# Optimization experiments

Hardware: AMD Instinct MI355X
Metric: run time of the kernel (lower is better)

## Reference

```python
import jax, jax.numpy as jnp
import numpy as np


def setup_inputs() -> dict:
    key = jax.random.key(0)
    B, S, N, D = 4, 512, 8, 256
    ks = jax.random.split(key, 5)
    s = 0.02
    inp = {"x": jax.random.normal(ks[0], (B, S, N, D), jnp.float32)}
    for k, name in zip(ks[1:], ["Wq", "Wk", "Wv", "Wo"]):
        inp[name] = jax.random.normal(k, (D, D), jnp.float32) * s
    for name in ["bq", "bk", "bv", "bo"]:
        inp[name] = jnp.zeros((D,), jnp.float32)
    inp["gamma"] = jnp.ones((D,), jnp.float32)
    inp["beta"] = jnp.zeros((D,), jnp.float32)
    inp["num_heads"] = 8
    return inp


def reference(x, Wq, bq, Wk, bk, Wv, bv, Wo, bo, gamma, beta, num_heads):
    B, S, N, D = x.shape
    H = num_heads
    hd = D // H
    # sinusoidal positional encoding: even dims sin, odd dims cos
    pos = jnp.arange(S, dtype=jnp.float32)[:, None]                      # (S,1)
    div = jnp.exp(jnp.arange(0, D, 2, dtype=jnp.float32) * (-np.log(10000.0) / D))
    ang = pos * div                                                       # (S, D/2)
    pe = jnp.stack([jnp.sin(ang), jnp.cos(ang)], axis=-1).reshape(S, D)   # (S, D)
    x_pos = x + pe[None, :, None, :]                                      # (B,S,N,D)
    # fold sensors into batch: (B*N, S, D)
    xr = x_pos.transpose(0, 2, 1, 3).reshape(B * N, S, D)

    def proj(W, b):
        y = xr @ W.T + b                                                  # torch Linear
        return y.reshape(B * N, S, H, hd).transpose(0, 2, 1, 3)          # (BN,H,S,hd)

    Q, K, V = proj(Wq, bq), proj(Wk, bk), proj(Wv, bv)
    scores = jnp.einsum('bhqd,bhkd->bhqk', Q, K) / np.sqrt(hd)            # (BN,H,S,S)
    causal = jnp.tril(jnp.ones((S, S), dtype=bool))
    scores = jnp.where(causal[None, None], scores, jnp.float32(-1e9))
    attn = jax.nn.softmax(scores, axis=-1)                                # dropout = eval mode
    out = jnp.einsum('bhqk,bhkd->bhqd', attn, V)                          # (BN,H,S,hd)
    out = out.transpose(0, 2, 1, 3).reshape(B * N, S, D)
    out = out @ Wo.T + bo
    out = out.reshape(B, N, S, D).transpose(0, 2, 1, 3)                   # (B,S,N,D)
    y = out + x
    mu = jnp.mean(y, axis=-1, keepdims=True)
    var = jnp.var(y, axis=-1, keepdims=True)
    return (y - mu) / jnp.sqrt(var + 1e-5) * gamma + beta
```

## Files before the change

### kernel.cpp

```cpp
#include <hip/hip_runtime.h>
#include <hip/hip_bf16.h>
#include <math.h>

#define B_   4
#define S_   512
#define N_   8
#define D_   256
#define H_   8
#define HD_  32
#define BN_  32
#define MTOT (BN_ * S_)

typedef __attribute__((ext_vector_type(8))) short short8;
typedef __attribute__((ext_vector_type(4))) short short4v;
typedef __attribute__((ext_vector_type(4))) float floatx4;

#define QSCALE 0.25503468f

__device__ __forceinline__ float bf2f(short u) {
    union { unsigned u; float f; } c;
    c.u = ((unsigned)(unsigned short)u) << 16;
    return c.f;
}
__device__ __forceinline__ unsigned short f2bf(float f) {
    union { float f; unsigned u; } c; c.f = f;
    unsigned lsb = (c.u >> 16) & 1u;
    c.u += 0x7fffu + lsb;
    return (unsigned short)(c.u >> 16);
}
__device__ __forceinline__ unsigned short f2bf_ru(float f) {
    union { float f; unsigned u; } c; c.f = f;
    return (unsigned short)((c.u + 0x8000u) >> 16);
}
__device__ __forceinline__ float fexp2(float x) {
    float r; asm("v_exp_f32 %0, %1" : "=v"(r) : "v"(x)); return r;
}

__global__ __launch_bounds__(256) void prep_kernel(const float* __restrict__ x,
                                                   const float* __restrict__ Wq,
                                                   const float* __restrict__ Wk,
                                                   const float* __restrict__ Wv,
                                                   const float* __restrict__ Wo,
                                                   unsigned short* __restrict__ xpos,
                                                   unsigned short* __restrict__ wdst) {
    int bid = blockIdx.x;
    if (bid < 4096) {
        int idx4 = bid * 256 + threadIdx.x;
        int d0 = (idx4 << 2) & (D_ - 1);
        int s  = (idx4 >> 6) & (S_ - 1);
        int bn = idx4 >> 15;
        int b = bn >> 3, n = bn & 7;
        floatx4 xv = *(const floatx4*)(x + ((((size_t)b * S_ + s) * N_ + n) << 8) + d0);
        const float cfreq = -9.210340371976184f / 256.0f;
        float f0 = __expf((float)d0 * cfreq);
        float f1 = __expf((float)(d0 + 2) * cfreq);
        float a0 = (float)s * f0, a1 = (float)s * f1;
        short4v o;
        o[0] = (short)f2bf(xv[0] + __sinf(a0));
        o[1] = (short)f2bf(xv[1] + __cosf(a0));
        o[2] = (short)f2bf(xv[2] + __sinf(a1));
        o[3] = (short)f2bf(xv[3] + __cosf(a1));
        *(short4v*)(xpos + ((size_t)idx4 << 2)) = o;
    } else {
        int idx = (bid - 4096) * 256 + threadIdx.x;
        int which = idx >> 16, off = idx & 65535;
        const float* W = (which == 0) ? Wq : (which == 1) ? Wk : (which == 2) ? Wv : Wo;
        wdst[idx] = f2bf(W[off]);
    }
}

__global__ __launch_bounds__(256) void gemm_qkv_kernel(const unsigned short* __restrict__ A,
                                                       const unsigned short* __restrict__ W,
                                                       const float* __restrict__ bq,
                                                       const float* __restrict__ bk,
                                                       const float* __restrict__ bv,
                                                       unsigned short* __restrict__ Qb,
                                                       unsigned short* __restrict__ Kb,
                                                       unsigned short* __restrict__ Vt) {
    int wv = threadIdx.x >> 6, lane = threadIdx.x & 63;
    int col = lane & 15, quad = lane >> 4;
    int m_w = blockIdx.x * 128 + (wv >> 1) * 64;
    int n_w = blockIdx.y * 128 + (wv & 1) * 64;

    const short8* Ap = (const short8*)(A + (size_t)(m_w + col) * 256 + quad * 8);
    const short8* Bp = (const short8*)(W + (size_t)(n_w + col) * 256 + quad * 8);

    floatx4 acc[4][4] = {};
#pragma unroll
    for (int kk = 0; kk < 8; ++kk) {
        short8 a[4], b[4];
#pragma unroll
        for (int t = 0; t < 4; ++t) {
            a[t] = Ap[t * 512 + kk * 4];
            b[t] = Bp[t * 512 + kk * 4];
        }
#pragma unroll
        for (int mt = 0; mt < 4; ++mt)
#pragma unroll
            for (int nt = 0; nt < 4; ++nt)
                acc[mt][nt] = __builtin_amdgcn_mfma_f32_16x16x32_bf16(a[mt], b[nt], acc[mt][nt], 0, 0, 0);
    }

    int sel = blockIdx.y >> 1;
    const float* bias = (sel == 0) ? bq : (sel == 1) ? bk : bv;
#pragma unroll
    for (int nt = 0; nt < 4; ++nt) {
        int c = n_w + nt * 16 + col - sel * 256;
        float bv_ = bias[c];
#pragma unroll
        for (int mt = 0; mt < 4; ++mt) {
            int m0 = m_w + mt * 16 + quad * 4;
            if (sel == 2) {
                int bn = m0 >> 9, s0 = m0 & (S_ - 1);
                short4v pack;
#pragma unroll
                for (int r = 0; r < 4; ++r) pack[r] = (short)f2bf(acc[mt][nt][r] + bv_);
                *(short4v*)(Vt + (((size_t)((bn << 8) + c)) << 9) + s0) = pack;
            } else if (sel == 0) {
#pragma unroll
                for (int r = 0; r < 4; ++r)
                    Qb[((size_t)(m0 + r) << 8) | c] = f2bf((acc[mt][nt][r] + bv_) * QSCALE);
            } else {
#pragma unroll
                for (int r = 0; r < 4; ++r)
                    Kb[((size_t)(m0 + r) << 8) | c] = f2bf(acc[mt][nt][r] + bv_);
            }
        }
    }
}

#define PSTR 40
__global__ __launch_bounds__(256) void fattn_kernel(const unsigned short* __restrict__ Q,
                                                    const unsigned short* __restrict__ K,
                                                    const unsigned short* __restrict__ Vt,
                                                    unsigned short* __restrict__ O) {
    __shared__ unsigned short Plds[4][16 * PSTR];
    int wv = threadIdx.x >> 6, lane = threadIdx.x & 63;
    int col = lane & 15, quad = lane >> 4;
    int bnh  = blockIdx.x & 255;
    int qblk = blockIdx.x >> 8;
    int bn = bnh >> 3, h = bnh & 7;
    int q0 = qblk * 64 + wv * 16;

    unsigned short* P = &Plds[wv][0];

    short8 qfrag = *(const short8*)(Q + (((size_t)(bn * S_ + q0 + col)) << 8) + h * HD_ + quad * 8);
    const unsigned short* Kbase = K + (((size_t)(bn * S_)) << 8) + h * HD_ + quad * 8;
    const unsigned short* Vbase = Vt + (((size_t)(bnh * HD_)) << 9) + quad * 8;

    float l = 0.f;
    floatx4 o0 = {0.f, 0.f, 0.f, 0.f};
    floatx4 o1 = {0.f, 0.f, 0.f, 0.f};
    int lastk = q0 >> 5;

    for (int kt = 0; kt <= lastk; ++kt) {
        int k0 = kt * 32;
        short8 kf0 = *(const short8*)(Kbase + ((size_t)(k0 + col) << 8));
        short8 kf1 = *(const short8*)(Kbase + ((size_t)(k0 + 16 + col) << 8));
        floatx4 z = {0.f, 0.f, 0.f, 0.f};
        floatx4 st0 = __builtin_amdgcn_mfma_f32_16x16x32_bf16(kf0, qfrag, z, 0, 0, 0);
        floatx4 st1 = __builtin_amdgcn_mfma_f32_16x16x32_bf16(kf1, qfrag, z, 0, 0, 0);

        if (kt == lastk) {
            int qg = q0 + col;
#pragma unroll
            for (int r = 0; r < 4; ++r) {
                if (k0 + quad * 4 + r > qg)      st0[r] = -1e30f;
                if (k0 + 16 + quad * 4 + r > qg) st1[r] = -1e30f;
            }
        }

        float p[8]; float ts = 0.f;
#pragma unroll
        for (int r = 0; r < 4; ++r) {
            p[r]     = fexp2(st0[r]);
            p[4 + r] = fexp2(st1[r]);
            ts += p[r] + p[4 + r];
        }
        ts += __shfl_xor(ts, 16);
        ts += __shfl_xor(ts, 32);
        l += ts;

        short4v pk0, pk1;
#pragma unroll
        for (int r = 0; r < 4; ++r) {
            pk0[r] = (short)f2bf_ru(p[r]);
            pk1[r] = (short)f2bf_ru(p[4 + r]);
        }
        *(short4v*)&P[col * PSTR + quad * 4]      = pk0;
        *(short4v*)&P[col * PSTR + 16 + quad * 4] = pk1;
        asm volatile("s_waitcnt lgkmcnt(0)" ::: "memory");
        short8 pfrag = *(const short8*)&P[col * PSTR + quad * 8];

        short8 vf0 = *(const short8*)(Vbase + ((size_t)col << 9) + k0);
        short8 vf1 = *(const short8*)(Vbase + ((size_t)(16 + col) << 9) + k0);
        o0 = __builtin_amdgcn_mfma_f32_16x16x32_bf16(vf0, pfrag, o0, 0, 0, 0);
        o1 = __builtin_amdgcn_mfma_f32_16x16x32_bf16(vf1, pfrag, o1, 0, 0, 0);
    }

    float inv = 1.0f / l;
    unsigned short* Op = O + (((size_t)(bn * S_ + q0 + col)) << 8) + h * HD_;
    short4v s0v, s1v;
#pragma unroll
    for (int r = 0; r < 4; ++r) {
        s0v[r] = (short)f2bf(o0[r] * inv);
        s1v[r] = (short)f2bf(o1[r] * inv);
    }
    *(short4v*)(Op + quad * 4)      = s0v;
    *(short4v*)(Op + 16 + quad * 4) = s1v;
}

__global__ __launch_bounds__(256) void gemm_o_ln_kernel(const unsigned short* __restrict__ A,
                                                        const unsigned short* __restrict__ W,
                                                        const float* __restrict__ bo,
                                                        const float* __restrict__ x,
                                                        const float* __restrict__ gamma,
                                                        const float* __restrict__ beta,
                                                        float* __restrict__ out) {
    __shared__ float lsum[4][64];
    __shared__ float lss[4][64];
    __shared__ float lmu[64];
    __shared__ float lrs[64];

    int wv = threadIdx.x >> 6, lane = threadIdx.x & 63;
    int col = lane & 15, quad = lane >> 4;
    int m_b = blockIdx.x * 64;
    int n_w = wv * 64;

    const short8* Ap = (const short8*)(A + (size_t)(m_b + col) * 256 + quad * 8);
    const short8* Bp = (const short8*)(W + (size_t)(n_w + col) * 256 + quad * 8);

    floatx4 acc[4][4] = {};
#pragma unroll
    for (int kk = 0; kk < 8; ++kk) {
        short8 a[4], b[4];
#pragma unroll
        for (int t = 0; t < 4; ++t) {
            a[t] = Ap[t * 512 + kk * 4];
            b[t] = Bp[t * 512 + kk * 4];
        }
#pragma unroll
        for (int mt = 0; mt < 4; ++mt)
#pragma unroll
            for (int nt = 0; nt < 4; ++nt)
                acc[mt][nt] = __builtin_amdgcn_mfma_f32_16x16x32_bf16(a[mt], b[nt], acc[mt][nt], 0, 0, 0);
    }

    int bn = m_b >> 9, s0 = m_b & (S_ - 1);
    int b_ = bn >> 3, n_ = bn & 7;
    const float* xrow = x + ((((size_t)b_ * S_ + s0) * N_ + n_) << 8);
    float* orow = out + ((((size_t)b_ * S_ + s0) * N_ + n_) << 8);

    float psum[4][4] = {};
    float pss[4][4]  = {};
#pragma unroll
    for (int nt = 0; nt < 4; ++nt) {
        int c = n_w + nt * 16 + col;
        float bv_ = bo[c];
#pragma unroll
        for (int mt = 0; mt < 4; ++mt) {
            int sl = mt * 16 + quad * 4;
#pragma unroll
            for (int r = 0; r < 4; ++r) {
                float y = acc[mt][nt][r] + bv_ + xrow[(size_t)(sl + r) * 2048 + c];
                acc[mt][nt][r] = y;
                psum[mt][r] += y;
                pss[mt][r]  += y * y;
            }
        }
    }
#pragma unroll
    for (int off = 8; off >= 1; off >>= 1) {
#pragma unroll
        for (int mt = 0; mt < 4; ++mt)
#pragma unroll
            for (int r = 0; r < 4; ++r) {
                psum[mt][r] += __shfl_xor(psum[mt][r], off);
                pss[mt][r]  += __shfl_xor(pss[mt][r], off);
            }
    }
    if (col == 0) {
#pragma unroll
        for (int mt = 0; mt < 4; ++mt)
#pragma unroll
            for (int r = 0; r < 4; ++r) {
                lsum[wv][mt * 16 + quad * 4 + r] = psum[mt][r];
                lss[wv][mt * 16 + quad * 4 + r]  = pss[mt][r];
            }
    }
    __syncthreads();
    if (threadIdx.x < 64) {
        int row = threadIdx.x;
        float s  = lsum[0][row] + lsum[1][row] + lsum[2][row] + lsum[3][row];
        float ss = lss[0][row] + lss[1][row] + lss[2][row] + lss[3][row];
        float mu = s * (1.0f / 256.0f);
        float var = ss * (1.0f / 256.0f) - mu * mu;
        lmu[row] = mu;
        lrs[row] = rsqrtf(var + 1e-5f);
    }
    __syncthreads();

#pragma unroll
    for (int nt = 0; nt < 4; ++nt) {
        int c = n_w + nt * 16 + col;
        float g  = gamma[c];
        float be = beta[c];
#pragma unroll
        for (int mt = 0; mt < 4; ++mt) {
            int sl = mt * 16 + quad * 4;
#pragma unroll
            for (int r = 0; r < 4; ++r)
                orow[(size_t)(sl + r) * 2048 + c] =
                    (acc[mt][nt][r] - lmu[sl + r]) * lrs[sl + r] * g + be;
        }
    }
}

extern "C" void kernel_launch(void* const* d_in, const int* in_sizes, int n_in,
                              void* d_out, int out_size, void* d_ws, size_t ws_size,
                              hipStream_t stream) {
    const float* x     = (const float*)d_in[0];
    const float* Wq    = (const float*)d_in[1];
    const float* Wk    = (const float*)d_in[2];
    const float* Wv    = (const float*)d_in[3];
    const float* Wo    = (const float*)d_in[4];
    const float* bq    = (const float*)d_in[5];
    const float* bk    = (const float*)d_in[6];
    const float* bv    = (const float*)d_in[7];
    const float* bo    = (const float*)d_in[8];
    const float* gamma = (const float*)d_in[9];
    const float* beta  = (const float*)d_in[10];

    char* w = (char*)d_ws;
    const size_t SZ = (size_t)MTOT * D_ * 2;
    unsigned short* xpos = (unsigned short*)(w);
    unsigned short* Qb   = (unsigned short*)(w + SZ);
    unsigned short* Kb   = (unsigned short*)(w + 2 * SZ);
    unsigned short* Vt   = (unsigned short*)(w + 3 * SZ);
    unsigned short* Ab   = (unsigned short*)(w + 4 * SZ);
    unsigned short* Wbf  = (unsigned short*)(w + 5 * SZ);

    prep_kernel<<<5120, 256, 0, stream>>>(x, Wq, Wk, Wv, Wo, xpos, Wbf);
    gemm_qkv_kernel<<<dim3(128, 6), 256, 0, stream>>>(xpos, Wbf, bq, bk, bv, Qb, Kb, Vt);
    fattn_kernel<<<2048, 256, 0, stream>>>(Qb, Kb, Vt, Ab);
    gemm_o_ln_kernel<<<256, 256, 0, stream>>>(Ab, Wbf + 3 * 65536, bo, x, gamma, beta, (float*)d_out);
}
```

Baseline: 167.7 us.

## Fuse all stages into one cooperative persistent kernel with grid syncs

Replaces the four separate launches (prep, QKV GEMM, flash attention, O-proj+LayerNorm) with a single cooperative kernel of 256 blocks of 1024 threads, separated by grid-wide syncs. Work is remapped per wave: the QKV GEMM uses 64x48 wave tiles, and attention pairs query tile i with tile 31-i so causal work is balanced across waves. The aim is to remove launch gaps and tail effects between stages. In exchange it adds grid-sync cost, and 1024-thread blocks limit occupancy and register budget.

New measurement: 280.0 us. 1.67x slower.

```diff
diff --git a/kernel.cpp b/kernel.cpp
--- a/kernel.cpp
+++ b/kernel.cpp
@@ -1,6 +1,9 @@
 #include <hip/hip_runtime.h>
 #include <hip/hip_bf16.h>
+#include <hip/hip_cooperative_groups.h>
 #include <math.h>
+
+namespace cg = cooperative_groups;
 
 #define B_   4
 #define S_   512
@@ -17,11 +20,6 @@
 
 #define QSCALE 0.25503468f
 
-__device__ __forceinline__ float bf2f(short u) {
-    union { unsigned u; float f; } c;
-    c.u = ((unsigned)(unsigned short)u) << 16;
-    return c.f;
-}
 __device__ __forceinline__ unsigned short f2bf(float f) {
     union { float f; unsigned u; } c; c.f = f;
     unsigned lsb = (c.u >> 16) & 1u;
@@ -36,282 +34,263 @@
     float r; asm("v_exp_f32 %0, %1" : "=v"(r) : "v"(x)); return r;
 }
 
-__global__ __launch_bounds__(256) void prep_kernel(const float* __restrict__ x,
-                                                   const float* __restrict__ Wq,
-                                                   const float* __restrict__ Wk,
-                                                   const float* __restrict__ Wv,
-                                                   const float* __restrict__ Wo,
-                                                   unsigned short* __restrict__ xpos,
-                                                   unsigned short* __restrict__ wdst) {
-    int bid = blockIdx.x;
-    if (bid < 4096) {
-        int idx4 = bid * 256 + threadIdx.x;
-        int d0 = (idx4 << 2) & (D_ - 1);
-        int s  = (idx4 >> 6) & (S_ - 1);
-        int bn = idx4 >> 15;
-        int b = bn >> 3, n = bn & 7;
-        floatx4 xv = *(const floatx4*)(x + ((((size_t)b * S_ + s) * N_ + n) << 8) + d0);
+#define PSTR 40
+
+__global__ __launch_bounds__(1024) void mega_kernel(
+        const float* __restrict__ x,
+        const float* __restrict__ Wq, const float* __restrict__ Wk,
+        const float* __restrict__ Wv, const float* __restrict__ Wo,
+        const float* __restrict__ bq, const float* __restrict__ bk,
+        const float* __restrict__ bv, const float* __restrict__ bo,
+        const float* __restrict__ gamma, const float* __restrict__ beta,
+        unsigned short* __restrict__ xpos, unsigned short* __restrict__ Wbf,
+        unsigned short* __restrict__ Qb, unsigned short* __restrict__ Kb,
+        unsigned short* __restrict__ Vt, unsigned short* __restrict__ Ab,
+        float* __restrict__ out) {
+    cg::grid_group grid = cg::this_grid();
+    __shared__ __align__(16) char smem[16 * 16 * PSTR * 2];
+
+    const int wid  = threadIdx.x >> 6;
+    const int lane = threadIdx.x & 63;
+    const int col  = lane & 15, quad = lane >> 4;
+    const int gw   = blockIdx.x * 16 + wid;
+    const int tid  = blockIdx.x * 1024 + threadIdx.x;
+
+    {
         const float cfreq = -9.210340371976184f / 256.0f;
-        float f0 = __expf((float)d0 * cfreq);
-        float f1 = __expf((float)(d0 + 2) * cfreq);
-        float a0 = (float)s * f0, a1 = (float)s * f1;
-        short4v o;
-        o[0] = (short)f2bf(xv[0] + __sinf(a0));
-        o[1] = (short)f2bf(xv[1] + __cosf(a0));
-        o[2] = (short)f2bf(xv[2] + __sinf(a1));
-        o[3] = (short)f2bf(xv[3] + __cosf(a1));
-        *(short4v*)(xpos + ((size_t)idx4 << 2)) = o;
-    } else {
-        int idx = (bid - 4096) * 256 + threadIdx.x;
-        int which = idx >> 16, off = idx & 65535;
+        for (int idx4 = tid; idx4 < (MTOT * D_) / 4; idx4 += 262144) {
+            int d0 = (idx4 << 2) & (D_ - 1);
+            int s  = (idx4 >> 6) & (S_ - 1);
+            int bn = idx4 >> 15;
+            int b = bn >> 3, n = bn & 7;
+            floatx4 xv = *(const floatx4*)(x + ((((size_t)b * S_ + s) * N_ + n) << 8) + d0);
+            float f0 = __expf((float)d0 * cfreq);
+            float f1 = __expf((float)(d0 + 2) * cfreq);
+            float a0 = (float)s * f0, a1 = (float)s * f1;
+            short4v o;
+            o[0] = (short)f2bf(xv[0] + __sinf(a0));
+            o[1] = (short)f2bf(xv[1] + __cosf(a0));
+            o[2] = (short)f2bf(xv[2] + __sinf(a1));
+            o[3] = (short)f2bf(xv[3] + __cosf(a1));
+            *(short4v*)(xpos + ((size_t)idx4 << 2)) = o;
+        }
+        int which = tid >> 16, off = tid & 65535;
         const float* W = (which == 0) ? Wq : (which == 1) ? Wk : (which == 2) ? Wv : Wo;
-        wdst[idx] = f2bf(W[off]);
+        Wbf[tid] = f2bf(W[off]);
     }
-}
-
-__global__ __launch_bounds__(256) void gemm_qkv_kernel(const unsigned short* __restrict__ A,
-                                                       const unsigned short* __restrict__ W,
-                                                       const float* __restrict__ bq,
-                                                       const float* __restrict__ bk,
-                                                       const float* __restrict__ bv,
-                                                       unsigned short* __restrict__ Qb,
-                                                       unsigned short* __restrict__ Kb,
-                                                       unsigned short* __restrict__ Vt) {
-    int wv = threadIdx.x >> 6, lane = threadIdx.x & 63;
-    int col = lane & 15, quad = lane >> 4;
-    int m_w = blockIdx.x * 128 + (wv >> 1) * 64;
-    int n_w = blockIdx.y * 128 + (wv & 1) * 64;
-
-    const short8* Ap = (const short8*)(A + (size_t)(m_w + col) * 256 + quad * 8);
-    const short8* Bp = (const short8*)(W + (size_t)(n_w + col) * 256 + quad * 8);
-
-    floatx4 acc[4][4] = {};
-#pragma unroll
-    for (int kk = 0; kk < 8; ++kk) {
-        short8 a[4], b[4];
-#pragma unroll
-        for (int t = 0; t < 4; ++t) {
-            a[t] = Ap[t * 512 + kk * 4];
-            b[t] = Bp[t * 512 + kk * 4];
-        }
-#pragma unroll
-        for (int mt = 0; mt < 4; ++mt)
+    grid.sync();
+
+    {
+        int m_idx = gw >> 4, n_idx = gw & 15;
+        int m_w = m_idx * 64, n_w = n_idx * 48;
+
+        const short8* Ap = (const short8*)(xpos + (size_t)(m_w + col) * 256 + quad * 8);
+        const short8* Bp = (const short8*)(Wbf + (size_t)(n_w + col) * 256 + quad * 8);
+
+        floatx4 acc[4][3] = {};
+#pragma unroll
+        for (int kk = 0; kk < 8; ++kk) {
+            short8 a[4], b[3];
+#pragma unroll
+            for (int t = 0; t < 4; ++t) a[t] = Ap[t * 512 + kk * 4];
+#pragma unroll
+            for (int t = 0; t < 3; ++t) b[t] = Bp[t * 512 + kk * 4];
+#pragma unroll
+            for (int mt = 0; mt < 4; ++mt)
+#pragma unroll
+                for (int nt = 0; nt < 3; ++nt)
+                    acc[mt][nt] = __builtin_amdgcn_mfma_f32_16x16x32_bf16(a[mt], b[nt], acc[mt][nt], 0, 0, 0);
+        }
+#pragma unroll
+        for (int nt = 0; nt < 3; ++nt) {
+            int cgl = n_w + nt * 16 + col;
+            int sel = cgl >> 8;
+            int c   = cgl & 255;
+            float bv_ = ((sel == 0) ? bq : (sel == 1) ? bk : bv)[c];
+#pragma unroll
+            for (int mt = 0; mt < 4; ++mt) {
+                int m0 = m_w + mt * 16 + quad * 4;
+                if (sel == 2) {
+                    int bn = m0 >> 9, s0 = m0 & (S_ - 1);
+                    short4v pack;
+#pragma unroll
+                    for (int r = 0; r < 4; ++r) pack[r] = (short)f2bf(acc[mt][nt][r] + bv_);
+                    *(short4v*)(Vt + (((size_t)((bn << 8) + c)) << 9) + s0) = pack;
+                } else if (sel == 0) {
+#pragma unroll
+                    for (int r = 0; r < 4; ++r)
+                        Qb[((size_t)(m0 + r) << 8) | c] = f2bf((acc[mt][nt][r] + bv_) * QSCALE);
+                } else {
+#pragma unroll
+                    for (int r = 0; r < 4; ++r)
+                        Kb[((size_t)(m0 + r) << 8) | c] = f2bf(acc[mt][nt][r] + bv_);
+                }
+            }
+        }
+    }
+    grid.sync();
+
+    {
+        unsigned short* P = (unsigned short*)smem + wid * (16 * PSTR);
+        int bnh = gw & 255;
+        int bn = bnh >> 3, h = bnh & 7;
+        int qts[2] = { gw >> 8, 31 - (gw >> 8) };
+        const unsigned short* Kbase = Kb + (((size_t)(bn * S_)) << 8) + h * HD_ + quad * 8;
+        const unsigned short* Vbase = Vt + (((size_t)(bnh * HD_)) << 9) + quad * 8;
+
+#pragma unroll
+        for (int ui = 0; ui < 2; ++ui) {
+            int q0 = qts[ui] * 16;
+            short8 qfrag = *(const short8*)(Qb + (((size_t)(bn * S_ + q0 + col)) << 8) + h * HD_ + quad * 8);
+            float l = 0.f;
+            floatx4 o0 = {0.f, 0.f, 0.f, 0.f};
+            floatx4 o1 = {0.f, 0.f, 0.f, 0.f};
+            int lastk = q0 >> 5;
+
+            for (int kt = 0; kt <= lastk; ++kt) {
+                int k0 = kt * 32;
+                short8 kf0 = *(const short8*)(Kbase + ((size_t)(k0 + col) << 8));
+                short8 kf1 = *(const short8*)(Kbase + ((size_t)(k0 + 16 + col) << 8));
+                floatx4 z = {0.f, 0.f, 0.f, 0.f};
+                floatx4 st0 = __builtin_amdgcn_mfma_f32_16x16x32_bf16(kf0, qfrag, z, 0, 0, 0);
+                floatx4 st1 = __builtin_amdgcn_mfma_f32_16x16x32_bf16(kf1, qfrag, z, 0, 0, 0);
+
+                if (kt == lastk) {
+                    int qg = q0 + col;
+#pragma unroll
+                    for (int r = 0; r < 4; ++r) {
+                        if (k0 + quad * 4 + r > qg)      st0[r] = -1e30f;
+                        if (k0 + 16 + quad * 4 + r > qg) st1[r] = -1e30f;
+                    }
+                }
+                float p[8]; float ts = 0.f;
+#pragma unroll
+                for (int r = 0; r < 4; ++r) {
+                    p[r]     = fexp2(st0[r]);
+                    p[4 + r] = fexp2(st1[r]);
+                    ts += p[r] + p[4 + r];
+                }
+                ts += __shfl_xor(ts, 16);
+                ts += __shfl_xor(ts, 32);
+                l += ts;
+
+                short4v pk0, pk1;
+#pragma unroll
+                for (int r = 0; r < 4; ++r) {
+                    pk0[r] = (short)f2bf_ru(p[r]);
+                    pk1[r] = (short)f2bf_ru(p[4 + r]);
+                }
+                *(short4v*)&P[col * PSTR + quad * 4]      = pk0;
+                *(short4v*)&P[col * PSTR + 16 + quad * 4] = pk1;
+                asm volatile("s_waitcnt lgkmcnt(0)" ::: "memory");
+                short8 pfrag = *(const short8*)&P[col * PSTR + quad * 8];
+
+                short8 vf0 = *(const short8*)(Vbase + ((size_t)col << 9) + k0);
+                short8 vf1 = *(const short8*)(Vbase + ((size_t)(16 + col) << 9) + k0);
+                o0 = __builtin_amdgcn_mfma_f32_16x16x32_bf16(vf0, pfrag, o0, 0, 0, 0);
+                o1 = __builtin_amdgcn_mfma_f32_16x16x32_bf16(vf1, pfrag, o1, 0, 0, 0);
+            }
+
+            float inv = 1.0f / l;
+            unsigned short* Op = Ab + (((size_t)(bn * S_ + q0 + col)) << 8) + h * HD_;
+            short4v s0v, s1v;
+#pragma unroll
+            for (int r = 0; r < 4; ++r) {
+                s0v[r] = (short)f2bf(o0[r] * inv);
+                s1v[r] = (short)f2bf(o1[r] * inv);
+            }
+            *(short4v*)(Op + quad * 4)      = s0v;
+            *(short4v*)(Op + 16 + quad * 4) = s1v;
+        }
+    }
+    grid.sync();
+
+    {
+        float* lsum = (float*)smem;
+        float* lss  = (float*)smem + 256;
+        float* lmu  = (float*)smem + 512;
+        float* lrs  = (float*)smem + 576;
+
+        const unsigned short* Wo_bf = Wbf + 3 * 65536;
+        int g  = wid >> 2, cq = wid & 3;
+        int m_b = blockIdx.x * 64;
+        int m_w = m_b + g * 16;
+        int n_w = cq * 64;
+
+        const short8* Ap = (const short8*)(Ab + (size_t)(m_w + col) * 256 + quad * 8);
+        const short8* Bp = (const short8*)(Wo_bf + (size_t)(n_w + col) * 256 + quad * 8);
+
+        floatx4 acc[4] = {};
+#pragma unroll
+        for (int kk = 0; kk < 8; ++kk) {
+            short8 a = Ap[kk * 4];
+            short8 b[4];
+#pragma unroll
+            for (int t = 0; t < 4; ++t) b[t] = Bp[t * 512 + kk * 4];
 #pragma unroll
             for (int nt = 0; nt < 4; ++nt)
-                acc[mt][nt] = __builtin_amdgcn_mfma_f32_16x16x32_bf16(a[mt], b[nt], acc[mt][nt], 0, 0, 0);
-    }
-
-    int sel = blockIdx.y >> 1;
-    const float* bias = (sel == 0) ? bq : (sel == 1) ? bk : bv;
-#pragma unroll
-    for (int nt = 0; nt < 4; ++nt) {
-        int c = n_w + nt * 16 + col - sel * 256;
-        float bv_ = bias[c];
-#pragma unroll
-        for (int mt = 0; mt < 4; ++mt) {
-            int m0 = m_w + mt * 16 + quad * 4;
-            if (sel == 2) {
-                int bn = m0 >> 9, s0 = m0 & (S_ - 1);
-                short4v pack;
-#pragma unroll
-                for (int r = 0; r < 4; ++r) pack[r] = (short)f2bf(acc[mt][nt][r] + bv_);
-                *(short4v*)(Vt + (((size_t)((bn << 8) + c)) << 9) + s0) = pack;
-            } else if (sel == 0) {
-#pragma unroll
-                for (int r = 0; r < 4; ++r)
-                    Qb[((size_t)(m0 + r) << 8) | c] = f2bf((acc[mt][nt][r] + bv_) * QSCALE);
-            } else {
-#pragma unroll
-                for (int r = 0; r < 4; ++r)
-                    Kb[((size_t)(m0 + r) << 8) | c] = f2bf(acc[mt][nt][r] + bv_);
-            }
-        }
-    }
-}
-
-#define PSTR 40
-__global__ __launch_bounds__(256) void fattn_kernel(const unsigned short* __restrict__ Q,
-                                                    const unsigned short* __restrict__ K,
-                                                    const unsigned short* __restrict__ Vt,
-                                                    unsigned short* __restrict__ O) {
-    __shared__ unsigned short Plds[4][16 * PSTR];
-    int wv = threadIdx.x >> 6, lane = threadIdx.x & 63;
-    int col = lane & 15, quad = lane >> 4;
-    int bnh  = blockIdx.x & 255;
-    int qblk = blockIdx.x >> 8;
-    int bn = bnh >> 3, h = bnh & 7;
-    int q0 = qblk * 64 + wv * 16;
-
-    unsigned short* P = &Plds[wv][0];
-
-    short8 qfrag = *(const short8*)(Q + (((size_t)(bn * S_ + q0 + col)) << 8) + h * HD_ + quad * 8);
-    const unsigned short* Kbase = K + (((size_t)(bn * S_)) << 8) + h * HD_ + quad * 8;
-    const unsigned short* Vbase = Vt + (((size_t)(bnh * HD_)) << 9) + quad * 8;
-
-    float l = 0.f;
-    floatx4 o0 = {0.f, 0.f, 0.f, 0.f};
-    floatx4 o1 = {0.f, 0.f, 0.f, 0.f};
-    int lastk = q0 >> 5;
-
-    for (int kt = 0; kt <= lastk; ++kt) {
-        int k0 = kt * 32;
-        short8 kf0 = *(const short8*)(Kbase + ((size_t)(k0 + col) << 8));
-        short8 kf1 = *(const short8*)(Kbase + ((size_t)(k0 + 16 + col) << 8));
-        floatx4 z = {0.f, 0.f, 0.f, 0.f};
-        floatx4 st0 = __builtin_amdgcn_mfma_f32_16x16x32_bf16(kf0, qfrag, z, 0, 0, 0);
-        floatx4 st1 = __builtin_amdgcn_mfma_f32_16x16x32_bf16(kf1, qfrag, z, 0, 0, 0);
-
-        if (kt == lastk) {
-            int qg = q0 + col;
-#pragma unroll
-            for (int r = 0; r < 4; ++r) {
-                if (k0 + quad * 4 + r > qg)      st0[r] = -1e30f;
-                if (k0 + 16 + quad * 4 + r > qg) st1[r] = -1e30f;
-            }
-        }
-
-        float p[8]; float ts = 0.f;
-#pragma unroll
-        for (int r = 0; r < 4; ++r) {
-            p[r]     = fexp2(st0[r]);
-            p[4 + r] = fexp2(st1[r]);
-            ts += p[r] + p[4 + r];
-        }
-        ts += __shfl_xor(ts, 16);
-        ts += __shfl_xor(ts, 32);
-        l += ts;
-
-        short4v pk0, pk1;
-#pragma unroll
-        for (int r = 0; r < 4; ++r) {
-            pk0[r] = (short)f2bf_ru(p[r]);
-            pk1[r] = (short)f2bf_ru(p[4 + r]);
-        }
-        *(short4v*)&P[col * PSTR + quad * 4]      = pk0;
-        *(short4v*)&P[col * PSTR + 16 + quad * 4] = pk1;
-        asm volatile("s_waitcnt lgkmcnt(0)" ::: "memory");
-        short8 pfrag = *(const short8*)&P[col * PSTR + quad * 8];
-
-        short8 vf0 = *(const short8*)(Vbase + ((size_t)col << 9) + k0);
-        short8 vf1 = *(const short8*)(Vbase + ((size_t)(16 + col) << 9) + k0);
-        o0 = __builtin_amdgcn_mfma_f32_16x16x32_bf16(vf0, pfrag, o0, 0, 0, 0);
-        o1 = __builtin_amdgcn_mfma_f32_16x16x32_bf16(vf1, pfrag, o1, 0, 0, 0);
-    }
-
-    float inv = 1.0f / l;
-    unsigned short* Op = O + (((size_t)(bn * S_ + q0 + col)) << 8) + h * HD_;
-    short4v s0v, s1v;
-#pragma unroll
-    for (int r = 0; r < 4; ++r) {
-        s0v[r] = (short)f2bf(o0[r] * inv);
-        s1v[r] = (short)f2bf(o1[r] * inv);
-    }
-    *(short4v*)(Op + quad * 4)      = s0v;
-    *(short4v*)(Op + 16 + quad * 4) = s1v;
-}
-
-__global__ __launch_bounds__(256) void gemm_o_ln_kernel(const unsigned short* __restrict__ A,
-                                                        const unsigned short* __restrict__ W,
-                                                        const float* __restrict__ bo,
-                                                        const float* __restrict__ x,
-                                                        const float* __restrict__ gamma,
-                                                        const float* __restrict__ beta,
-                                                        float* __restrict__ out) {
-    __shared__ float lsum[4][64];
-    __shared__ float lss[4][64];
-    __shared__ float lmu[64];
-    __shared__ float lrs[64];
-
-    int wv = threadIdx.x >> 6, lane = threadIdx.x & 63;
-    int col = lane & 15, quad = lane >> 4;
-    int m_b = blockIdx.x * 64;
-    int n_w = wv * 64;
-
-    const short8* Ap = (const short8*)(A + (size_t)(m_b + col) * 256 + quad * 8);
-    const short8* Bp = (const short8*)(W + (size_t)(n_w + col) * 256 + quad * 8);
-
-    floatx4 acc[4][4] = {};
-#pragma unroll
-    for (int kk = 0; kk < 8; ++kk) {
-        short8 a[4], b[4];
-#pragma unroll
-        for (int t = 0; t < 4; ++t) {
-            a[t] = Ap[t * 512 + kk * 4];
-            b[t] = Bp[t * 512 + kk * 4];
-        }
-#pragma unroll
-        for (int mt = 0; mt < 4; ++mt)
-#pragma unroll
-            for (int nt = 0; nt < 4; ++nt)
-                acc[mt][nt] = __builtin_amdgcn_mfma_f32_16x16x32_bf16(a[mt], b[nt], acc[mt][nt], 0, 0, 0);
-    }
-
-    int bn = m_b >> 9, s0 = m_b & (S_ - 1);
-    int b_ = bn >> 3, n_ = bn & 7;
-    const float* xrow = x + ((((size_t)b_ * S_ + s0) * N_ + n_) << 8);
-    float* orow = out + ((((size_t)b_ * S_ + s0) * N_ + n_) << 8);
-
-    float psum[4][4] = {};
-    float pss[4][4]  = {};
-#pragma unroll
-    for (int nt = 0; nt < 4; ++nt) {
-        int c = n_w + nt * 16 + col;
-        float bv_ = bo[c];
-#pragma unroll
-        for (int mt = 0; mt < 4; ++mt) {
-            int sl = mt * 16 + quad * 4;
-#pragma unroll
-            for (int r = 0; r < 4; ++r) {
-                float y = acc[mt][nt][r] + bv_ + xrow[(size_t)(sl + r) * 2048 + c];
-                acc[mt][nt][r] = y;
-                psum[mt][r] += y;
-                pss[mt][r]  += y * y;
-            }
-        }
-    }
-#pragma unroll
-    for (int off = 8; off >= 1; off >>= 1) {
-#pragma unroll
-        for (int mt = 0; mt < 4; ++mt)
-#pragma unroll
-            for (int r = 0; r < 4; ++r) {
-                psum[mt][r] += __shfl_xor(psum[mt][r], off);
-                pss[mt][r]  += __shfl_xor(pss[mt][r], off);
-            }
-    }
-    if (col == 0) {
-#pragma unroll
-        for (int mt = 0; mt < 4; ++mt)
-#pragma unroll
-            for (int r = 0; r < 4; ++r) {
-                lsum[wv][mt * 16 + quad * 4 + r] = psum[mt][r];
-                lss[wv][mt * 16 + quad * 4 + r]  = pss[mt][r];
-            }
-    }
-    __syncthreads();
-    if (threadIdx.x < 64) {
-        int row = threadIdx.x;
-        float s  = lsum[0][row] + lsum[1][row] + lsum[2][row] + lsum[3][row];
-        float ss = lss[0][row] + lss[1][row] + lss[2][row] + lss[3][row];
-        float mu = s * (1.0f / 256.0f);
-        float var = ss * (1.0f / 256.0f) - mu * mu;
-        lmu[row] = mu;
-        lrs[row] = rsqrtf(var + 1e-5f);
-    }
-    __syncthreads();
-
-#pragma unroll
-    for (int nt = 0; nt < 4; ++nt) {
-        int c = n_w + nt * 16 + col;
-        float g  = gamma[c];
-        float be = beta[c];
-#pragma unroll
-        for (int mt = 0; mt < 4; ++mt) {
-            int sl = mt * 16 + quad * 4;
-#pragma unroll
-            for (int r = 0; r < 4; ++r)
-                orow[(size_t)(sl + r) * 2048 + c] =
-                    (acc[mt][nt][r] - lmu[sl + r]) * lrs[sl + r] * g + be;
+                acc[nt] = __builtin_amdgcn_mfma_f32_16x16x32_bf16(a, b[nt], acc[nt], 0, 0, 0);
+        }
+
+        int bn = m_b >> 9, s0 = m_b & (S_ - 1);
+        int b_ = bn >> 3, n_ = bn & 7;
+        const float* xrow = x + ((((size_t)b_ * S_ + s0) * N_ + n_) << 8);
+        float* orow = out + ((((size_t)b_ * S_ + s0) * N_ + n_) << 8);
+
+        float psum[4] = {}, pss[4] = {};
+#pragma unroll
+        for (int nt = 0; nt < 4; ++nt) {
+            int c = n_w + nt * 16 + col;
+            float bv_ = bo[c];
+#pragma unroll
+            for (int r = 0; r < 4; ++r) {
+                int sl = g * 16 + quad * 4 + r;
+                float y = acc[nt][r] + bv_ + xrow[(size_t)sl * 2048 + c];
+                acc[nt][r] = y;
+                psum[r] += y;
+                pss[r]  += y * y;
+            }
+        }
+#pragma unroll
+        for (int off = 8; off >= 1; off >>= 1) {
+#pragma unroll
+            for (int r = 0; r < 4; ++r) {
+                psum[r] += __shfl_xor(psum[r], off);
+                pss[r]  += __shfl_xor(pss[r], off);
+            }
+        }
+        if (col == 0) {
+#pragma unroll
+            for (int r = 0; r < 4; ++r) {
+                lsum[wid * 16 + quad * 4 + r] = psum[r];
+                lss[wid * 16 + quad * 4 + r]  = pss[r];
+            }
+        }
+        __syncthreads();
+        if (threadIdx.x < 64) {
+            int row = threadIdx.x;
+            int gg = row >> 4, rl = row & 15;
+            float s = 0.f, ss = 0.f;
+#pragma unroll
+            for (int q2 = 0; q2 < 4; ++q2) {
+                s  += lsum[(gg * 4 + q2) * 16 + rl];
+                ss += lss[(gg * 4 + q2) * 16 + rl];
+            }
+            float mu = s * (1.0f / 256.0f);
+            float var = ss * (1.0f / 256.0f) - mu * mu;
+            lmu[row] = mu;
+            lrs[row] = rsqrtf(var + 1e-5f);
+        }
+        __syncthreads();
+#pragma unroll
+        for (int nt = 0; nt < 4; ++nt) {
+            int c = n_w + nt * 16 + col;
+            float ga = gamma[c], be = beta[c];
+#pragma unroll
+            for (int r = 0; r < 4; ++r) {
+                int sl = g * 16 + quad * 4 + r;
+                orow[(size_t)sl * 2048 + c] = (acc[nt][r] - lmu[sl]) * lrs[sl] * ga + be;
+            }
         }
     }
 }
@@ -339,9 +318,10 @@
     unsigned short* Vt   = (unsigned short*)(w + 3 * SZ);
     unsigned short* Ab   = (unsigned short*)(w + 4 * SZ);
     unsigned short* Wbf  = (unsigned short*)(w + 5 * SZ);
-
-    prep_kernel<<<5120, 256, 0, stream>>>(x, Wq, Wk, Wv, Wo, xpos, Wbf);
-    gemm_qkv_kernel<<<dim3(128, 6), 256, 0, stream>>>(xpos, Wbf, bq, bk, bv, Qb, Kb, Vt);
-    fattn_kernel<<<2048, 256, 0, stream>>>(Qb, Kb, Vt, Ab);
-    gemm_o_ln_kernel<<<256, 256, 0, stream>>>(Ab, Wbf + 3 * 65536, bo, x, gamma, beta, (float*)d_out);
-}
+    float* outp = (float*)d_out;
+
+    void* args[] = { &x, &Wq, &Wk, &Wv, &Wo, &bq, &bk, &bv, &bo, &gamma, &beta,
+                     &xpos, &Wbf, &Qb, &Kb, &Vt, &Ab, &outp };
+    hipLaunchCooperativeKernel((const void*)mega_kernel, dim3(256), dim3(1024),
+                               args, 0, stream);
+}
```
